# Kernel tuning notes

Hardware: AMD Instinct MI355X
Metric: run time of the kernel (lower is better)

## Reference

```python
import jax, jax.numpy as jnp
import numpy as np

N = 50000   # nodes
E = 1600000 # edges
G = 256     # graphs
EPS = 1e-5  # batchnorm eps (torch default)


def _bn(h, g, b):
    # training-mode BatchNorm1d: biased batch stats
    m = h.mean(0)
    v = h.var(0)
    return (h - m) * jax.lax.rsqrt(v + EPS) * g + b


def _mlp(h, W1, b1, g, be, W2, b2):
    # Lin -> BN -> ReLU -> Lin
    h = jax.nn.relu(_bn(h @ W1 + b1, g, be))
    return h @ W2 + b2


def _scatter_mean(v, idx, n):
    s = jax.ops.segment_sum(v, idx, num_segments=n)
    c = jax.ops.segment_sum(jnp.ones((v.shape[0], 1), v.dtype), idx, num_segments=n)
    return s / jnp.maximum(c, 1.0)


def setup_inputs() -> dict:
    key = jax.random.key(0)
    ks = iter(jax.random.split(key, 32))
    d = {}
    d["x"] = jax.random.normal(next(ks), (N, 48), dtype=jnp.float32)
    d["edge_index"] = jax.random.randint(next(ks), (2, E), 0, N, dtype=jnp.int64)
    d["batch"] = jnp.sort(jax.random.randint(next(ks), (N,), 0, G, dtype=jnp.int64))

    def lin(k, fin, fout):
        kw, kb = jax.random.split(k)
        s = 1.0 / np.sqrt(fin)
        return (jax.random.uniform(kw, (fin, fout), jnp.float32, -s, s),
                jax.random.uniform(kb, (fout,), jnp.float32, -s, s))

    # input BatchNorm1d(48)
    d["bn_g"] = jnp.ones((48,), jnp.float32)
    d["bn_b"] = jnp.zeros((48,), jnp.float32)

    def mlp_params(prefix, fin, fmid, fout):
        W1, b1 = lin(next(ks), fin, fmid)
        W2, b2 = lin(next(ks), fmid, fout)
        d[prefix + "_W1"], d[prefix + "_b1"] = W1, b1
        d[prefix + "_g"] = jnp.ones((fmid,), jnp.float32)
        d[prefix + "_be"] = jnp.zeros((fmid,), jnp.float32)
        d[prefix + "_W2"], d[prefix + "_b2"] = W2, b2

    mlp_params("e", 96, 128, 128)    # EdgeBlock
    mlp_params("n1", 176, 128, 128)  # NodeBlock mlp1
    mlp_params("n2", 176, 128, 128)  # NodeBlock mlp2
    mlp_params("gl", 128, 128, 2)    # GlobalBlock
    return d


def reference(x, edge_index, batch, bn_g, bn_b,
              e_W1, e_b1, e_g, e_be, e_W2, e_b2,
              n1_W1, n1_b1, n1_g, n1_be, n1_W2, n1_b2,
              n2_W1, n2_b1, n2_g, n2_be, n2_W2, n2_b2,
              gl_W1, gl_b1, gl_g, gl_be, gl_W2, gl_b2):
    x = _bn(x, bn_g, bn_b)
    row, col = edge_index[0], edge_index[1]
    # EdgeBlock: cat(src, dest) -> MLP
    edge_attr = _mlp(jnp.concatenate([x[row], x[col]], axis=1),
                     e_W1, e_b1, e_g, e_be, e_W2, e_b2)
    # NodeBlock: cat(x[row], edge_attr) -> mlp1 -> scatter_mean(col) -> cat(x,.) -> mlp2
    m = _mlp(jnp.concatenate([x[row], edge_attr], axis=1),
             n1_W1, n1_b1, n1_g, n1_be, n1_W2, n1_b2)
    agg = _scatter_mean(m, col, N)
    x2 = _mlp(jnp.concatenate([x, agg], axis=1),
              n2_W1, n2_b1, n2_g, n2_be, n2_W2, n2_b2)
    # GlobalBlock: scatter_mean over graphs -> MLP -> [G, 2]
    u = _scatter_mean(x2, batch, G)
    u = _mlp(u, gl_W1, gl_b1, gl_g, gl_be, gl_W2, gl_b2)
    return u
```

## Files before the change

kernel.cpp:

```cpp
#include <hip/hip_runtime.h>
#include <hip/hip_bf16.h>
#include <stdint.h>

#define DEV static __device__ __forceinline__

constexpr int N_ = 50000;
constexpr int E_ = 1600000;
constexpr int G_ = 256;

typedef __attribute__((ext_vector_type(8))) short short8;
typedef __attribute__((ext_vector_type(4))) float float4v;

DEV uint16_t f2bf(float f){
  uint32_t u = __float_as_uint(f);
  uint32_t r = (u + 0x7fffu + ((u >> 16) & 1u)) >> 16;
  return (uint16_t)r;
}
DEV float bf2f(uint16_t v){ return __uint_as_float((uint32_t)v << 16); }
DEV void unpack2(uint32_t p, float& a, float& b){
  a = __uint_as_float(p << 16);
  b = __uint_as_float(p & 0xffff0000u);
}
DEV uint32_t pack2(float a, float b){
  return (uint32_t)f2bf(a) | ((uint32_t)f2bf(b) << 16);
}
DEV short8 lds_load8(const uint16_t* p){
  union { short8 v; uint2 u[2]; } c;
  c.u[0] = *(const uint2*)p;
  c.u[1] = *(const uint2*)(p + 4);
  return c.v;
}
DEV void lds_store16B_as8(uint32_t* d, uint4 v){
  *(uint2*)d       = make_uint2(v.x, v.y);
  *(uint2*)(d + 2) = make_uint2(v.z, v.w);
}

__global__ __launch_bounds__(256) void k_xstats(const float* __restrict__ x, float* __restrict__ xstats){
  __shared__ float lst[96];
  int t = threadIdx.x;
  if (t < 96) lst[t] = 0.f;
  __syncthreads();
  int gid = blockIdx.x * 256 + t;
  int c4 = (gid % 12) * 4;
  float s[4] = {0,0,0,0}, q[4] = {0,0,0,0};
  const float4v* x4 = (const float4v*)x;
  for (int i = gid; i < N_ * 12; i += 64512){
    float4v v = x4[i];
    #pragma unroll
    for (int j = 0; j < 4; j++){ s[j] += v[j]; q[j] += v[j]*v[j]; }
  }
  #pragma unroll
  for (int j = 0; j < 4; j++){
    atomicAdd(&lst[c4 + j], s[j]);
    atomicAdd(&lst[48 + c4 + j], q[j]);
  }
  __syncthreads();
  if (t < 96) atomicAdd(&xstats[t], lst[t]);
}

__global__ void k_xfin(const float* __restrict__ xstats, const float* __restrict__ g,
                       const float* __restrict__ b, float* __restrict__ sx, float* __restrict__ tx){
  int c = threadIdx.x;
  if (c < 48){
    float m = xstats[c] / (float)N_;
    float v = xstats[48 + c] / (float)N_ - m*m;
    float s = g[c] / sqrtf(v + 1e-5f);
    sx[c] = s; tx[c] = b[c] - m*s;
  }
}

__global__ __launch_bounds__(256) void k_hist(const int* __restrict__ ei, int* __restrict__ counts){
  int e = blockIdx.x * 256 + threadIdx.x;
  if (e < E_) atomicAdd(&counts[ei[E_ + e]], 1);
}

__global__ __launch_bounds__(256) void k_invc(const int* __restrict__ counts, float* __restrict__ invc){
  int n = blockIdx.x * 256 + threadIdx.x;
  if (n < N_){ int c = counts[n]; invc[n] = (c > 0) ? 1.f/(float)c : 0.f; }
}

__global__ __launch_bounds__(256) void k_scanA(const int* __restrict__ counts, int* __restrict__ bsum){
  __shared__ int ws[4];
  int b = blockIdx.x, t = threadIdx.x, lane = t & 63, w = t >> 6;
  int i0 = b*1024 + t*4;
  int s = 0;
  #pragma unroll
  for (int j = 0; j < 4; j++){ int i = i0 + j; if (i < N_) s += counts[i]; }
  for (int d = 1; d < 64; d <<= 1) s += __shfl_xor(s, d);
  if (lane == 0) ws[w] = s;
  __syncthreads();
  if (t == 0) bsum[b] = ws[0] + ws[1] + ws[2] + ws[3];
}
__global__ void k_scanB(const int* __restrict__ bsum, int* __restrict__ boff, int* __restrict__ off, int nb){
  int t = threadIdx.x;
  int v = (t < nb) ? bsum[t] : 0;
  int x = v;
  for (int d = 1; d < 64; d <<= 1){ int y = __shfl_up(x, d); if (t >= d) x += y; }
  if (t < nb) boff[t] = x - v;
  if (t == 63) off[N_] = x;
}
__global__ __launch_bounds__(256) void k_scanC(const int* __restrict__ counts, const int* __restrict__ boff,
                                               int* __restrict__ off, int* __restrict__ cur){
  __shared__ int ws[4];
  int b = blockIdx.x, t = threadIdx.x, lane = t & 63, w = t >> 6;
  int i0 = b*1024 + t*4;
  int v0 = (i0+0 < N_) ? counts[i0+0] : 0;
  int v1 = (i0+1 < N_) ? counts[i0+1] : 0;
  int v2 = (i0+2 < N_) ? counts[i0+2] : 0;
  int v3 = (i0+3 < N_) ? counts[i0+3] : 0;
  int ts = v0+v1+v2+v3, xs = ts;
  for (int d = 1; d < 64; d <<= 1){ int y = __shfl_up(xs, d); if (lane >= d) xs += y; }
  if (lane == 63) ws[w] = xs;
  __syncthreads();
  int woff = 0;
  for (int k = 0; k < w; k++) woff += ws[k];
  int excl = xs - ts + woff + boff[b];
  int e0 = excl, e1 = e0+v0, e2 = e1+v1, e3 = e2+v2;
  if (i0+0 < N_){ off[i0+0] = e0; cur[i0+0] = e0; }
  if (i0+1 < N_){ off[i0+1] = e1; cur[i0+1] = e1; }
  if (i0+2 < N_){ off[i0+2] = e2; cur[i0+2] = e2; }
  if (i0+3 < N_){ off[i0+3] = e3; cur[i0+3] = e3; }
}

__global__ __launch_bounds__(256) void k_place(const int* __restrict__ ei, int* __restrict__ cur,
                                               int2* __restrict__ rcs){
  int e = blockIdx.x * 256 + threadIdx.x;
  if (e < E_){
    int c = ei[E_ + e];
    int p = atomicAdd(&cur[c], 1);
    rcs[p] = make_int2(ei[e], c);
  }
}

__global__ __launch_bounds__(256) void k_wprep(
    const float* __restrict__ eW2, const float* __restrict__ n1W1,
    const float* __restrict__ n1W2, const float* __restrict__ n2W1,
    const float* __restrict__ n2W2, const float* __restrict__ glW1,
    const float* __restrict__ n1b2, const float* __restrict__ n2b2,
    uint16_t* __restrict__ Mt, float* __restrict__ Wcomb,
    float* __restrict__ M3, float* __restrict__ c1, float* __restrict__ c3){
  int flat = blockIdx.x * 256 + threadIdx.x;
  if (flat < 16384){
    int n = flat & 127, k = flat >> 7;
    float a = 0.f;
    for (int j = 0; j < 128; j++) a += eW2[k*128 + j] * n1W1[(48 + j)*128 + n];
    Mt[n*128 + k] = f2bf(a);
  } else if (flat < 32768){
    int b = flat - 16384;
    int n = b & 127, j = b >> 7;
    float a = 0.f;
    for (int m = 0; m < 128; m++) a += n1W2[j*128 + m] * n2W1[(48 + m)*128 + n];
    Wcomb[(48 + j)*128 + n] = a;
  } else if (flat < 38912){
    int b = flat - 32768;
    int n = b & 127, k = b >> 7;
    Wcomb[k*128 + n] = n2W1[k*128 + n];
  } else if (flat < 55296){
    int b = flat - 38912;
    int n = b & 127, j = b >> 7;
    float a = 0.f;
    for (int m = 0; m < 128; m++) a += n2W2[j*128 + m] * glW1[m*128 + n];
    M3[j*128 + n] = a;
  } else if (flat < 55552){
    int e = flat - 55296;
    if (e < 128){
      float a = 0.f;
      for (int m = 0; m < 128; m++) a += n1b2[m] * n2W1[(48 + m)*128 + e];
      c1[e] = a;
    } else {
      int n = e - 128;
      float a = 0.f;
      for (int m = 0; m < 128; m++) a += n2b2[m] * glW1[m*128 + n];
      c3[n] = a;
    }
  }
}

__global__ __launch_bounds__(256) void k_nodegemm(
    const float* __restrict__ x, const float* __restrict__ sx, const float* __restrict__ tx,
    const float* __restrict__ eW1, const float* __restrict__ n1W1,
    uint16_t* __restrict__ AC, uint16_t* __restrict__ Bn){
  __shared__ float xT[48][36];
  __shared__ float W[48][128];
  int t = threadIdx.x;
  int n0 = blockIdx.x * 32;
  for (int idx = t; idx < 384; idx += 256){
    int r = idx / 12, q = idx % 12;
    int n = n0 + r;
    float4v v = {0.f,0.f,0.f,0.f};
    if (n < N_) v = *(const float4v*)&x[(size_t)n*48 + q*4];
    #pragma unroll
    for (int i = 0; i < 4; i++){
      int k = q*4 + i;
      xT[k][r] = v[i] * sx[k] + tx[k];
    }
  }
  int cg = t & 31, ng = t >> 5;
  const float* Wsrc0 = eW1;
  const float* Wsrc1 = eW1 + 48*128;
  const float* Wsrc2 = n1W1;
  for (int seg = 0; seg < 3; seg++){
    const float* Wsrc = (seg == 0) ? Wsrc0 : (seg == 1) ? Wsrc1 : Wsrc2;
    __syncthreads();
    {
      const float4v* src4 = (const float4v*)Wsrc;
      float4v* W4 = (float4v*)W;
      for (int idx = t; idx < 1536; idx += 256) W4[idx] = src4[idx];
    }
    __syncthreads();
    float acc[4][4] = {{0.f}};
    #pragma unroll 4
    for (int k = 0; k < 48; k++){
      float4v xv = *(const float4v*)&xT[k][ng*4];
      float4v wv = *(const float4v*)&W[k][cg*4];
      #pragma unroll
      for (int i = 0; i < 4; i++)
        #pragma unroll
        for (int j = 0; j < 4; j++)
          acc[i][j] += xv[i]*wv[j];
    }
    #pragma unroll
    for (int i = 0; i < 4; i++){
      int n = n0 + ng*4 + i;
      if (n >= N_) continue;
      uint2 pv;
      pv.x = pack2(acc[i][0], acc[i][1]);
      pv.y = pack2(acc[i][2], acc[i][3]);
      if (seg == 0)      *(uint2*)&AC[(size_t)n*256 + cg*4] = pv;
      else if (seg == 1) *(uint2*)&Bn[(size_t)n*128 + cg*4] = pv;
      else               *(uint2*)&AC[(size_t)n*256 + 128 + cg*4] = pv;
    }
  }
}

__global__ __launch_bounds__(256) void k_estats(const int2* __restrict__ rcs,
    const uint16_t* __restrict__ AC, const uint16_t* __restrict__ Bn, float* __restrict__ estR){
  __shared__ float red[4][64][4];
  __shared__ float lst[256];
  int t = threadIdx.x, lane = t & 63, w = t >> 6;
  int wid = blockIdx.x * 4 + w, nw = gridDim.x * 4;
  float s0=0,q0=0,s1=0,q1=0;
  const uint32_t* ACu = (const uint32_t*)AC;
  const uint32_t* Bu  = (const uint32_t*)Bn;
  for (int e = wid; e < E_; e += nw){
    int2 rc = rcs[e];
    uint32_t pa = ACu[(size_t)rc.x*128 + lane];
    uint32_t pb = Bu[(size_t)rc.y*64 + lane];
    float a0,a1,b0,b1; unpack2(pa,a0,a1); unpack2(pb,b0,b1);
    float h0 = a0 + b0, h1 = a1 + b1;
    s0 += h0; q0 += h0*h0; s1 += h1; q1 += h1*h1;
  }
  red[w][lane][0]=s0; red[w][lane][1]=q0; red[w][lane][2]=s1; red[w][lane][3]=q1;
  __syncthreads();
  if (t < 64){
    float S0=0,Q0=0,S1=0,Q1=0;
    for (int ww = 0; ww < 4; ww++){ S0+=red[ww][t][0]; Q0+=red[ww][t][1]; S1+=red[ww][t][2]; Q1+=red[ww][t][3]; }
    lst[2*t] = S0; lst[2*t+1] = S1; lst[128+2*t] = Q0; lst[128+2*t+1] = Q1;
  }
  __syncthreads();
  atomicAdd(&estR[(blockIdx.x & 63)*256 + t], lst[t]);
}

__global__ void k_bnfin(const float* __restrict__ statsR, int reps, const float* __restrict__ g,
                        const float* __restrict__ be, float* __restrict__ s_out, float* __restrict__ t_out,
                        float inv_n){
  int c = threadIdx.x;
  if (c >= 128) return;
  float sm = 0.f, sq = 0.f;
  for (int r = 0; r < reps; r++){ sm += statsR[r*256 + c]; sq += statsR[r*256 + 128 + c]; }
  float m = sm * inv_n;
  float v = sq * inv_n - m*m;
  float s = g[c] / sqrtf(v + 1e-5f);
  s_out[c] = s;
  t_out[c] = be[c] - m*s;
}


__global__ __launch_bounds__(256) void k_epass0(
    const int2* __restrict__ rcs,
    const uint16_t* __restrict__ AC, const uint16_t* __restrict__ Bn,
    const uint16_t* __restrict__ Mt, const float* __restrict__ se, const float* __restrict__ te,
    float* __restrict__ n1R){
  __shared__ __align__(16) uint16_t bufA[64*132];
  __shared__ __align__(16) uint16_t bufB[128*132];
  __shared__ __align__(16) float sete[256];
  __shared__ float lst[256];
  const int t = threadIdx.x;
  const long i0 = (long)blockIdx.x * 64;
  const int lane = t & 63, w = t >> 6;
  const int m = lane & 15, quad = lane >> 4;
  const int e = t >> 2, q = t & 3;

  int2 rc = rcs[i0 + e];
  const uint4* Ap = (const uint4*)((const uint32_t*)AC + (size_t)rc.x*128 + q*16);
  const uint4* Bp = (const uint4*)((const uint32_t*)Bn + (size_t)rc.y*64  + q*16);
  const uint4* Cp = (const uint4*)((const uint32_t*)AC + (size_t)rc.x*128 + 64 + q*16);
  uint4 va0 = Ap[0], va1 = Ap[1], va2 = Ap[2], va3 = Ap[3];
  uint4 vb0 = Bp[0], vb1 = Bp[1], vb2 = Bp[2], vb3 = Bp[3];
  uint4 vc0 = Cp[0], vc1 = Cp[1], vc2 = Cp[2], vc3 = Cp[3];

  if (t < 128){ sete[t] = se[t]; sete[128 + t] = te[t]; }
  lst[t] = 0.f;
  __syncthreads();

  {
    uint32_t* dstd = (uint32_t*)bufA + e*66 + q*16;
    int cb = q*32;
    uint4 vas[4] = {va0, va1, va2, va3};
    uint4 vbs[4] = {vb0, vb1, vb2, vb3};
    #pragma unroll
    for (int u = 0; u < 4; u++){
      uint4 va = vas[u], vb = vbs[u];
      float4v sA = *(const float4v*)&sete[cb + u*8];
      float4v sB = *(const float4v*)&sete[cb + u*8 + 4];
      float4v tA = *(const float4v*)&sete[128 + cb + u*8];
      float4v tB = *(const float4v*)&sete[128 + cb + u*8 + 4];
      float a0,a1,b0,b1; uint4 o;
      unpack2(va.x,a0,a1); unpack2(vb.x,b0,b1);
      o.x = pack2(fmaxf(0.f,(a0+b0)*sA[0]+tA[0]), fmaxf(0.f,(a1+b1)*sA[1]+tA[1]));
      unpack2(va.y,a0,a1); unpack2(vb.y,b0,b1);
      o.y = pack2(fmaxf(0.f,(a0+b0)*sA[2]+tA[2]), fmaxf(0.f,(a1+b1)*sA[3]+tA[3]));
      unpack2(va.z,a0,a1); unpack2(vb.z,b0,b1);
      o.z = pack2(fmaxf(0.f,(a0+b0)*sB[0]+tB[0]), fmaxf(0.f,(a1+b1)*sB[1]+tB[1]));
      unpack2(va.w,a0,a1); unpack2(vb.w,b0,b1);
      o.w = pack2(fmaxf(0.f,(a0+b0)*sB[2]+tB[2]), fmaxf(0.f,(a1+b1)*sB[3]+tB[3]));
      lds_store16B_as8(dstd + u*4, o);
    }
  }
  {
    int n = t >> 1, h = t & 1;
    const uint4* src = (const uint4*)((const uint32_t*)Mt + n*64 + h*32);
    uint32_t* dstd = (uint32_t*)bufB + n*66 + h*32;
    #pragma unroll
    for (int u = 0; u < 8; u++) lds_store16B_as8(dstd + u*4, src[u]);
  }
  __syncthreads();

  float4v acc[8];
  #pragma unroll
  for (int nt = 0; nt < 8; nt++){ acc[nt][0]=0.f; acc[nt][1]=0.f; acc[nt][2]=0.f; acc[nt][3]=0.f; }
  {
    const uint16_t* aptr = bufA + (w*16 + m)*132 + quad*8;
    const uint16_t* bbase = bufB + m*132 + quad*8;
    #pragma unroll
    for (int ks = 0; ks < 4; ks++){
      short8 af = lds_load8(aptr + ks*32);
      #pragma unroll
      for (int nt = 0; nt < 8; nt++){
        short8 bf = lds_load8(bbase + nt*16*132 + ks*32);
        acc[nt] = __builtin_amdgcn_mfma_f32_16x16x32_bf16(af, bf, acc[nt], 0, 0, 0);
      }
    }
  }
  __syncthreads();

  {
    uint32_t* dstd = (uint32_t*)bufA + e*66 + q*16;
    lds_store16B_as8(dstd + 0,  vc0);
    lds_store16B_as8(dstd + 4,  vc1);
    lds_store16B_as8(dstd + 8,  vc2);
    lds_store16B_as8(dstd + 12, vc3);
  }
  #pragma unroll
  for (int nt = 0; nt < 8; nt++)
    #pragma unroll
    for (int reg = 0; reg < 4; reg++)
      bufB[(w*16 + quad*4 + reg)*132 + nt*16 + m] = f2bf(acc[nt][reg]);
  __syncthreads();

  {
    int cp = t & 63, eg = t >> 6;
    float ss0=0,qq0=0,ss1=0,qq1=0;
    #pragma unroll
    for (int it = 0; it < 16; it++){
      int ee = it*4 + eg;
      uint32_t ph = ((uint32_t*)bufB)[ee*66 + cp];
      uint32_t pc = ((uint32_t*)bufA)[ee*66 + cp];
      float h0,h1,c0,c1v;
      unpack2(ph,h0,h1); unpack2(pc,c0,c1v);
      float v0 = h0 + c0, v1 = h1 + c1v;
      ss0 += v0; qq0 += v0*v0; ss1 += v1; qq1 += v1*v1;
    }
    atomicAdd(&lst[2*cp], ss0);
    atomicAdd(&lst[2*cp+1], ss1);
    atomicAdd(&lst[128+2*cp], qq0);
    atomicAdd(&lst[128+2*cp+1], qq1);
  }
  __syncthreads();
  atomicAdd(&n1R[(blockIdx.x & 63)*256 + t], lst[t]);
}

__global__ __launch_bounds__(256) void k_epass1(
    const int2* __restrict__ rcs,
    const uint16_t* __restrict__ AC, const uint16_t* __restrict__ Bn,
    const uint16_t* __restrict__ Mt, const float* __restrict__ se, const float* __restrict__ te,
    const float* __restrict__ sn1, const float* __restrict__ tn1,
    float* __restrict__ aggf){
  __shared__ __align__(16) uint16_t bufA[64*132];
  __shared__ __align__(16) uint16_t bufB[128*132];
  __shared__ __align__(16) float sete[256];
  __shared__ int ssid_s[64], scseg_s[64];
  __shared__ int snseg;
  const int t = threadIdx.x;
  const long i0 = (long)blockIdx.x * 64;
  const int lane = t & 63, w = t >> 6;
  const int m = lane & 15, quad = lane >> 4;
  const int e = t >> 2, q = t & 3;

  uint32_t* bufBu = (uint32_t*)bufB;
  float* segacc = (float*)(bufBu + 4224);

  int2 rc = rcs[i0 + e];
  const uint4* Ap = (const uint4*)((const uint32_t*)AC + (size_t)rc.x*128 + q*16);
  const uint4* Bp = (const uint4*)((const uint32_t*)Bn + (size_t)rc.y*64  + q*16);
  const uint4* Cp = (const uint4*)((const uint32_t*)AC + (size_t)rc.x*128 + 64 + q*16);
  uint4 va0 = Ap[0], va1 = Ap[1], va2 = Ap[2], va3 = Ap[3];
  uint4 vb0 = Bp[0], vb1 = Bp[1], vb2 = Bp[2], vb3 = Bp[3];
  uint4 vc0 = Cp[0], vc1 = Cp[1], vc2 = Cp[2], vc3 = Cp[3];

  if (t < 128){ sete[t] = se[t]; sete[128 + t] = te[t]; }
  if (t < 64){
    int myc = rcs[i0 + t].y;
    int prevc = (t > 0) ? rcs[i0 + t - 1].y : myc;
    bool bnd = (t > 0) && (myc != prevc);
    unsigned long long mask = __ballot(bnd);
    int sid = __popcll(mask << (63 - t));
    ssid_s[t] = sid;
    if (bnd || t == 0) scseg_s[sid] = myc;
    if (t == 63) snseg = sid + 1;
  }
  __syncthreads();

  {
    uint32_t* dstd = (uint32_t*)bufA + e*66 + q*16;
    int cb = q*32;
    uint4 vas[4] = {va0, va1, va2, va3};
    uint4 vbs[4] = {vb0, vb1, vb2, vb3};
    #pragma unroll
    for (int u = 0; u < 4; u++){
      uint4 va = vas[u], vb = vbs[u];
      float4v sA = *(const float4v*)&sete[cb + u*8];
      float4v sB = *(const float4v*)&sete[cb + u*8 + 4];
      float4v tA = *(const float4v*)&sete[128 + cb + u*8];
      float4v tB = *(const float4v*)&sete[128 + cb + u*8 + 4];
      float a0,a1,b0,b1; uint4 o;
      unpack2(va.x,a0,a1); unpack2(vb.x,b0,b1);
      o.x = pack2(fmaxf(0.f,(a0+b0)*sA[0]+tA[0]), fmaxf(0.f,(a1+b1)*sA[1]+tA[1]));
      unpack2(va.y,a0,a1); unpack2(vb.y,b0,b1);
      o.y = pack2(fmaxf(0.f,(a0+b0)*sA[2]+tA[2]), fmaxf(0.f,(a1+b1)*sA[3]+tA[3]));
      unpack2(va.z,a0,a1); unpack2(vb.z,b0,b1);
      o.z = pack2(fmaxf(0.f,(a0+b0)*sB[0]+tB[0]), fmaxf(0.f,(a1+b1)*sB[1]+tB[1]));
      unpack2(va.w,a0,a1); unpack2(vb.w,b0,b1);
      o.w = pack2(fmaxf(0.f,(a0+b0)*sB[2]+tB[2]), fmaxf(0.f,(a1+b1)*sB[3]+tB[3]));
      lds_store16B_as8(dstd + u*4, o);
    }
  }
  {
    int n = t >> 1, h = t & 1;
    const uint4* src = (const uint4*)((const uint32_t*)Mt + n*64 + h*32);
    uint32_t* dstd = bufBu + n*66 + h*32;
    #pragma unroll
    for (int u = 0; u < 8; u++) lds_store16B_as8(dstd + u*4, src[u]);
  }
  __syncthreads();

  float4v acc[8];
  #pragma unroll
  for (int nt = 0; nt < 8; nt++){ acc[nt][0]=0.f; acc[nt][1]=0.f; acc[nt][2]=0.f; acc[nt][3]=0.f; }
  {
    const uint16_t* aptr = bufA + (w*16 + m)*132 + quad*8;
    const uint16_t* bbase = bufB + m*132 + quad*8;
    #pragma unroll
    for (int ks = 0; ks < 4; ks++){
      short8 af = lds_load8(aptr + ks*32);
      #pragma unroll
      for (int nt = 0; nt < 8; nt++){
        short8 bf = lds_load8(bbase + nt*16*132 + ks*32);
        acc[nt] = __builtin_amdgcn_mfma_f32_16x16x32_bf16(af, bf, acc[nt], 0, 0, 0);
      }
    }
  }
  __syncthreads();

  {
    uint32_t* dstd = (uint32_t*)bufA + e*66 + q*16;
    lds_store16B_as8(dstd + 0,  vc0);
    lds_store16B_as8(dstd + 4,  vc1);
    lds_store16B_as8(dstd + 8,  vc2);
    lds_store16B_as8(dstd + 12, vc3);
  }
  #pragma unroll
  for (int nt = 0; nt < 8; nt++)
    #pragma unroll
    for (int reg = 0; reg < 4; reg++)
      bufB[(w*16 + quad*4 + reg)*132 + nt*16 + m] = f2bf(acc[nt][reg]);
  if (t < 128){ sete[t] = sn1[t]; sete[128 + t] = tn1[t]; }
  for (int i = t; i < 24*128; i += 256) segacc[i] = 0.f;
  __syncthreads();

  {
    int cp = t & 63, eg = t >> 6;
    float s0 = sete[2*cp], s1 = sete[2*cp+1];
    float b0 = sete[128+2*cp], b1 = sete[128+2*cp+1];
    int nseg = snseg;
    bool lp = (nseg <= 24);
    int cursid = ssid_s[eg*16];
    float r0 = 0.f, r1 = 0.f;
    for (int it = 0; it < 16; it++){
      int ee = eg*16 + it;
      uint32_t ph = bufBu[ee*66 + cp];
      uint32_t pc = ((uint32_t*)bufA)[ee*66 + cp];
      float h0,h1,c0,c1v;
      unpack2(ph,h0,h1); unpack2(pc,c0,c1v);
      float v0 = fmaxf(0.f, (h0+c0)*s0 + b0);
      float v1 = fmaxf(0.f, (h1+c1v)*s1 + b1);
      int sid = ssid_s[ee];
      if (sid != cursid){
        if (lp){ atomicAdd(&segacc[cursid*128 + 2*cp], r0); atomicAdd(&segacc[cursid*128 + 2*cp+1], r1); }
        else { int c = scseg_s[cursid];
               atomicAdd(&aggf[(size_t)c*128 + 2*cp], r0); atomicAdd(&aggf[(size_t)c*128 + 2*cp+1], r1); }
        cursid = sid; r0 = 0.f; r1 = 0.f;
      }
      r0 += v0; r1 += v1;
    }
    if (lp){ atomicAdd(&segacc[cursid*128 + 2*cp], r0); atomicAdd(&segacc[cursid*128 + 2*cp+1], r1); }
    else { int c = scseg_s[cursid];
           atomicAdd(&aggf[(size_t)c*128 + 2*cp], r0); atomicAdd(&aggf[(size_t)c*128 + 2*cp+1], r1); }
    __syncthreads();
    if (lp){
      for (int idx = t; idx < nseg*64; idx += 256){
        int s = idx >> 6, cpp = idx & 63;
        float v0 = segacc[s*128 + 2*cpp], v1 = segacc[s*128 + 2*cpp+1];
        int c = scseg_s[s];
        float* dst = &aggf[(size_t)c*128 + 2*cpp];
        if (s == 0 || s == nseg - 1){ atomicAdd(dst, v0); atomicAdd(dst+1, v1); }
        else { dst[0] = v0; dst[1] = v1; }
      }
    }
  }
}

__global__ __launch_bounds__(256) void k_n2(const float* __restrict__ x,
    const float* __restrict__ sx, const float* __restrict__ tx,
    const float* __restrict__ aggf, const float* __restrict__ invc,
    const float* __restrict__ Wc, const float* __restrict__ c1, const int* __restrict__ counts,
    float* __restrict__ hn2, float* __restrict__ n2R){
  __shared__ float xT[44][36];
  __shared__ float wT[44][128];
  __shared__ float lst[256];
  int t = threadIdx.x;
  int n0 = blockIdx.x * 32;
  int cg = t & 31, ng = t >> 5;
  lst[t] = 0.f;
  float acc[4][4] = {{0.f}};
  for (int kc = 0; kc < 176; kc += 44){
    __syncthreads();
    for (int idx = t; idx < 32*44; idx += 256){
      int r = idx / 44, k = idx % 44;
      int n = n0 + r, kk = kc + k;
      float v = 0.f;
      if (n < N_){
        if (kk < 48) v = x[(size_t)n*48 + kk] * sx[kk] + tx[kk];
        else         v = aggf[(size_t)n*128 + (kk - 48)] * invc[n];
      }
      xT[k][r] = v;
    }
    for (int idx = t; idx < 44*128; idx += 256){
      int k = idx >> 7, c = idx & 127;
      wT[k][c] = Wc[(kc + k)*128 + c];
    }
    __syncthreads();
    for (int k = 0; k < 44; k++){
      float4v xv = *(const float4v*)&xT[k][ng*4];
      float4v wv = *(const float4v*)&wT[k][cg*4];
      #pragma unroll
      for (int i = 0; i < 4; i++)
        #pragma unroll
        for (int j = 0; j < 4; j++)
          acc[i][j] += xv[i]*wv[j];
    }
  }
  float csum[4] = {0,0,0,0}, cqs[4] = {0,0,0,0};
  for (int i = 0; i < 4; i++){
    int n = n0 + ng*4 + i;
    if (n >= N_) continue;
    bool ok = counts[n] > 0;
    float4v o;
    #pragma unroll
    for (int j = 0; j < 4; j++){
      float vv = acc[i][j] + (ok ? c1[cg*4 + j] : 0.f);
      o[j] = vv; csum[j] += vv; cqs[j] += vv*vv;
    }
    *(float4v*)&hn2[(size_t)n*128 + cg*4] = o;
  }
  #pragma unroll
  for (int j = 0; j < 4; j++){
    atomicAdd(&lst[cg*4 + j], csum[j]);
    atomicAdd(&lst[128 + cg*4 + j], cqs[j]);
  }
  __syncthreads();
  atomicAdd(&n2R[(blockIdx.x & 63)*256 + t], lst[t]);
}

__global__ void k_goff(const int* __restrict__ batch, int* __restrict__ goff){
  int g = threadIdx.x;
  int lo = 0, hi = N_;
  while (lo < hi){ int mid = (lo + hi) >> 1; if (batch[mid] < g) lo = mid + 1; else hi = mid; }
  goff[g] = lo;
  if (g == 0) goff[256] = N_;
}

__global__ __launch_bounds__(128) void k_gmean(const float* __restrict__ hn2, const int* __restrict__ goff,
    const float* __restrict__ sn2, const float* __restrict__ tn2, float* __restrict__ gmean){
  int g = blockIdx.x, c = threadIdx.x;
  int b = goff[g], e = goff[g+1];
  float s = sn2[c], tt = tn2[c], a = 0.f;
  for (int r = b; r < e; r++) a += fmaxf(0.f, hn2[(size_t)r*128 + c]*s + tt);
  gmean[g*128 + c] = (e > b) ? a/(float)(e - b) : 0.f;
}

__global__ __launch_bounds__(256) void k_hg(const float* __restrict__ gmean, const float* __restrict__ M3,
    const float* __restrict__ c3, const int* __restrict__ goff,
    float* __restrict__ hg, float* __restrict__ gls){
  int idx = blockIdx.x * 256 + threadIdx.x;
  int g = idx >> 7, c = idx & 127;
  float a = 0.f;
  for (int k = 0; k < 128; k++) a += gmean[g*128 + k] * M3[k*128 + c];
  if (goff[g+1] > goff[g]) a += c3[c];
  hg[idx] = a;
  atomicAdd(&gls[c], a);
  atomicAdd(&gls[128 + c], a*a);
}

__global__ __launch_bounds__(256) void k_out(const float* __restrict__ hg, const float* __restrict__ sgl,
    const float* __restrict__ tgl, const float* __restrict__ glW2, const float* __restrict__ glb2,
    float* __restrict__ out){
  int idx = blockIdx.x * 256 + threadIdx.x;
  int g = idx >> 1, o = idx & 1;
  float a = 0.f;
  for (int c = 0; c < 128; c++){
    float r = fmaxf(0.f, hg[g*128 + c]*sgl[c] + tgl[c]);
    a += r * glW2[c*2 + o];
  }
  out[idx] = a + glb2[o];
}

extern "C" void kernel_launch(void* const* d_in, const int* in_sizes, int n_in,
                              void* d_out, int out_size, void* d_ws, size_t ws_size,
                              hipStream_t stream){
  const float* x     = (const float*)d_in[0];
  const int*   ei    = (const int*)d_in[1];
  const int*   batch = (const int*)d_in[2];
  const float* bn_g  = (const float*)d_in[3];
  const float* bn_b  = (const float*)d_in[4];
  const float* eW1   = (const float*)d_in[5];
  const float* e_g   = (const float*)d_in[7];
  const float* e_be  = (const float*)d_in[8];
  const float* eW2   = (const float*)d_in[9];
  const float* n1W1  = (const float*)d_in[11];
  const float* n1_g  = (const float*)d_in[13];
  const float* n1_be = (const float*)d_in[14];
  const float* n1W2  = (const float*)d_in[15];
  const float* n1b2  = (const float*)d_in[16];
  const float* n2W1  = (const float*)d_in[17];
  const float* n2_g  = (const float*)d_in[19];
  const float* n2_be = (const float*)d_in[20];
  const float* n2W2  = (const float*)d_in[21];
  const float* n2b2  = (const float*)d_in[22];
  const float* glW1  = (const float*)d_in[23];
  const float* gl_g  = (const float*)d_in[25];
  const float* gl_be = (const float*)d_in[26];
  const float* glW2  = (const float*)d_in[27];
  const float* glb2  = (const float*)d_in[28];
  float* out = (float*)d_out;

  char* w = (char*)d_ws;
  size_t off = 0;
  auto take = [&](size_t bytes) -> char* {
    char* p = w + off;
    off = (off + bytes + 511) & ~(size_t)511;
    return p;
  };

  const size_t ZONE_WORDS = 96 + 3*64*256 + 256 + N_;
  float* zone   = (float*)take(ZONE_WORDS * 4);
  float* xstats = zone;
  float* estR   = zone + 96;
  float* n1R    = zone + 96 + 64*256;
  float* n2R    = zone + 96 + 2*64*256;
  float* gls    = zone + 96 + 3*64*256;
  int*   counts = (int*)(zone + 96 + 3*64*256 + 256);

  float* sx = (float*)take(48*4);   float* tx = (float*)take(48*4);
  float* se = (float*)take(128*4);  float* te = (float*)take(128*4);
  float* sn1 = (float*)take(128*4); float* tn1 = (float*)take(128*4);
  float* sn2 = (float*)take(128*4); float* tn2 = (float*)take(128*4);
  float* sgl = (float*)take(128*4); float* tgl = (float*)take(128*4);
  float* c1 = (float*)take(128*4);  float* c3 = (float*)take(128*4);
  float* invc  = (float*)take((size_t)N_*4);
  float* Wcomb = (float*)take(176*128*4);
  float* M3    = (float*)take(128*128*4);
  float* gmean = (float*)take(G_*128*4);
  float* hg    = (float*)take(G_*128*4);
  int* offs = (int*)take((N_+1)*4);
  int* cur  = (int*)take(N_*4);
  int* goff = (int*)take(257*4);
  int* bsum = (int*)take(64*4);
  int* boff = (int*)take(64*4);
  uint16_t* Mt = (uint16_t*)take(128*128*2);
  uint16_t* AC = (uint16_t*)take((size_t)N_*256*2);
  uint16_t* Bn = (uint16_t*)take((size_t)N_*128*2);
  float* aggf  = (float*)take((size_t)N_*128*4);
  float* hn2   = (float*)take((size_t)N_*128*4);
  int2* rcs = (int2*)take((size_t)E_*8);

  if (off > ws_size) return;

  hipMemsetAsync(zone, 0, ZONE_WORDS*4, stream);
  hipMemsetAsync(aggf, 0, (size_t)N_*128*4, stream);

  const int NB = (N_ + 1023) / 1024;
  hipLaunchKernelGGL(k_xstats, dim3(252), dim3(256), 0, stream, x, xstats);
  hipLaunchKernelGGL(k_hist, dim3((E_+255)/256), dim3(256), 0, stream, ei, counts);
  hipLaunchKernelGGL(k_xfin, dim3(1), dim3(64), 0, stream, xstats, bn_g, bn_b, sx, tx);
  hipLaunchKernelGGL(k_scanA, dim3(NB), dim3(256), 0, stream, counts, bsum);
  hipLaunchKernelGGL(k_scanB, dim3(1), dim3(64), 0, stream, bsum, boff, offs, NB);
  hipLaunchKernelGGL(k_scanC, dim3(NB), dim3(256), 0, stream, counts, boff, offs, cur);
  hipLaunchKernelGGL(k_place, dim3((E_+255)/256), dim3(256), 0, stream, ei, cur, rcs);
  hipLaunchKernelGGL(k_invc, dim3((N_+255)/256), dim3(256), 0, stream, counts, invc);
  hipLaunchKernelGGL(k_wprep, dim3(217), dim3(256), 0, stream,
                     eW2, n1W1, n1W2, n2W1, n2W2, glW1, n1b2, n2b2, Mt, Wcomb, M3, c1, c3);
  hipLaunchKernelGGL(k_nodegemm, dim3((N_+31)/32), dim3(256), 0, stream,
                     x, sx, tx, eW1, n1W1, AC, Bn);
  hipLaunchKernelGGL(k_estats, dim3(1024), dim3(256), 0, stream, rcs, AC, Bn, estR);
  hipLaunchKernelGGL(k_bnfin, dim3(1), dim3(128), 0, stream, estR, 64, e_g, e_be, se, te, 1.f/(float)E_);
  hipLaunchKernelGGL(k_epass0, dim3(E_/64), dim3(256), 0, stream,
                     rcs, AC, Bn, Mt, se, te, n1R);
  hipLaunchKernelGGL(k_bnfin, dim3(1), dim3(128), 0, stream, n1R, 64, n1_g, n1_be, sn1, tn1, 1.f/(float)E_);
  hipLaunchKernelGGL(k_epass1, dim3(E_/64), dim3(256), 0, stream,
                     rcs, AC, Bn, Mt, se, te, sn1, tn1, aggf);
  hipLaunchKernelGGL(k_n2, dim3((N_+31)/32), dim3(256), 0, stream,
                     x, sx, tx, aggf, invc, Wcomb, c1, counts, hn2, n2R);
  hipLaunchKernelGGL(k_bnfin, dim3(1), dim3(128), 0, stream, n2R, 64, n2_g, n2_be, sn2, tn2, 1.f/(float)N_);
  hipLaunchKernelGGL(k_goff, dim3(1), dim3(256), 0, stream, batch, goff);
  hipLaunchKernelGGL(k_gmean, dim3(256), dim3(128), 0, stream, hn2, goff, sn2, tn2, gmean);
  hipLaunchKernelGGL(k_hg, dim3(128), dim3(256), 0, stream, gmean, M3, c3, goff, hg, gls);
  hipLaunchKernelGGL(k_bnfin, dim3(1), dim3(128), 0, stream, gls, 1, gl_g, gl_be, sgl, tgl, 1.f/(float)G_);
  hipLaunchKernelGGL(k_out, dim3(2), dim3(256), 0, stream, hg, sgl, tgl, glW2, glb2, out);
}
```

Measured before the change: 1.524 ms.

## Recompute per-edge row projections from gathered bf16 node features via MFMA

Node-level precomputed projections (AC, 256 bf16 per node) are replaced by a compact bf16 normalized-feature array (48 per node). Each edge kernel now gathers these 48-wide rows and recomputes the x[row]@W1 and x[row]@n1W1 products with MFMA inside the edge kernels. The dest-side term Bn is loaded once per column segment into LDS. The aim is to cut random-gather bandwidth over 1.6M edges at the cost of extra tensor-core compute in three edge passes. Blocks grow to 128 edges and 512 threads, and the edge-stats pass becomes an MFMA kernel.

```diff
diff --git a/kernel.cpp b/kernel.cpp
--- a/kernel.cpp
+++ b/kernel.cpp
@@ -29,10 +29,6 @@
   c.u[0] = *(const uint2*)p;
   c.u[1] = *(const uint2*)(p + 4);
   return c.v;
-}
-DEV void lds_store16B_as8(uint32_t* d, uint4 v){
-  *(uint2*)d       = make_uint2(v.x, v.y);
-  *(uint2*)(d + 2) = make_uint2(v.z, v.w);
 }
 
 __global__ __launch_bounds__(256) void k_xstats(const float* __restrict__ x, float* __restrict__ xstats){
@@ -133,12 +129,13 @@
 }
 
 __global__ __launch_bounds__(256) void k_wprep(
-    const float* __restrict__ eW2, const float* __restrict__ n1W1,
+    const float* __restrict__ eW1, const float* __restrict__ eW2, const float* __restrict__ n1W1,
     const float* __restrict__ n1W2, const float* __restrict__ n2W1,
     const float* __restrict__ n2W2, const float* __restrict__ glW1,
     const float* __restrict__ n1b2, const float* __restrict__ n2b2,
     uint16_t* __restrict__ Mt, float* __restrict__ Wcomb,
-    float* __restrict__ M3, float* __restrict__ c1, float* __restrict__ c3){
+    float* __restrict__ M3, float* __restrict__ c1, float* __restrict__ c3,
+    uint16_t* __restrict__ W1t, uint16_t* __restrict__ N1t){
   int flat = blockIdx.x * 256 + threadIdx.x;
   if (flat < 16384){
     int n = flat & 127, k = flat >> 7;
@@ -173,13 +170,21 @@
       for (int m = 0; m < 128; m++) a += n2b2[m] * glW1[m*128 + n];
       c3[n] = a;
     }
+  } else if (flat < 63744){
+    int b = flat - 55552;
+    int n = b & 127, k = b >> 7;
+    W1t[n*64 + k] = (k < 48) ? f2bf(eW1[k*128 + n]) : (uint16_t)0;
+  } else if (flat < 71936){
+    int b = flat - 63744;
+    int n = b & 127, j = b >> 7;
+    N1t[n*64 + j] = (j < 48) ? f2bf(n1W1[j*128 + n]) : (uint16_t)0;
   }
 }
 
 __global__ __launch_bounds__(256) void k_nodegemm(
     const float* __restrict__ x, const float* __restrict__ sx, const float* __restrict__ tx,
-    const float* __restrict__ eW1, const float* __restrict__ n1W1,
-    uint16_t* __restrict__ AC, uint16_t* __restrict__ Bn){
+    const float* __restrict__ eW1,
+    uint16_t* __restrict__ Bn, uint16_t* __restrict__ xn){
   __shared__ float xT[48][36];
   __shared__ float W[48][128];
   int t = threadIdx.x;
@@ -189,76 +194,47 @@
     int n = n0 + r;
     float4v v = {0.f,0.f,0.f,0.f};
     if (n < N_) v = *(const float4v*)&x[(size_t)n*48 + q*4];
+    float xv[4];
     #pragma unroll
     for (int i = 0; i < 4; i++){
       int k = q*4 + i;
-      xT[k][r] = v[i] * sx[k] + tx[k];
-    }
-  }
+      xv[i] = v[i] * sx[k] + tx[k];
+      xT[k][r] = xv[i];
+    }
+    if (n < N_){
+      uint2 pv;
+      pv.x = pack2(xv[0], xv[1]);
+      pv.y = pack2(xv[2], xv[3]);
+      *(uint2*)&xn[(size_t)n*48 + q*4] = pv;
+    }
+  }
+  {
+    const float4v* src4 = (const float4v*)(eW1 + 48*128);
+    float4v* W4 = (float4v*)W;
+    for (int idx = t; idx < 1536; idx += 256) W4[idx] = src4[idx];
+  }
+  __syncthreads();
   int cg = t & 31, ng = t >> 5;
-  const float* Wsrc0 = eW1;
-  const float* Wsrc1 = eW1 + 48*128;
-  const float* Wsrc2 = n1W1;
-  for (int seg = 0; seg < 3; seg++){
-    const float* Wsrc = (seg == 0) ? Wsrc0 : (seg == 1) ? Wsrc1 : Wsrc2;
-    __syncthreads();
-    {
-      const float4v* src4 = (const float4v*)Wsrc;
-      float4v* W4 = (float4v*)W;
-      for (int idx = t; idx < 1536; idx += 256) W4[idx] = src4[idx];
-    }
-    __syncthreads();
-    float acc[4][4] = {{0.f}};
-    #pragma unroll 4
-    for (int k = 0; k < 48; k++){
-      float4v xv = *(const float4v*)&xT[k][ng*4];
-      float4v wv = *(const float4v*)&W[k][cg*4];
-      #pragma unroll
-      for (int i = 0; i < 4; i++)
-        #pragma unroll
-        for (int j = 0; j < 4; j++)
-          acc[i][j] += xv[i]*wv[j];
-    }
-    #pragma unroll
-    for (int i = 0; i < 4; i++){
-      int n = n0 + ng*4 + i;
-      if (n >= N_) continue;
-      uint2 pv;
-      pv.x = pack2(acc[i][0], acc[i][1]);
-      pv.y = pack2(acc[i][2], acc[i][3]);
-      if (seg == 0)      *(uint2*)&AC[(size_t)n*256 + cg*4] = pv;
-      else if (seg == 1) *(uint2*)&Bn[(size_t)n*128 + cg*4] = pv;
-      else               *(uint2*)&AC[(size_t)n*256 + 128 + cg*4] = pv;
-    }
-  }
-}
-
-__global__ __launch_bounds__(256) void k_estats(const int2* __restrict__ rcs,
-    const uint16_t* __restrict__ AC, const uint16_t* __restrict__ Bn, float* __restrict__ estR){
-  __shared__ float red[4][64][4];
-  __shared__ float lst[256];
-  int t = threadIdx.x, lane = t & 63, w = t >> 6;
-  int wid = blockIdx.x * 4 + w, nw = gridDim.x * 4;
-  float s0=0,q0=0,s1=0,q1=0;
-  const uint32_t* ACu = (const uint32_t*)AC;
-  const uint32_t* Bu  = (const uint32_t*)Bn;
-  for (int e = wid; e < E_; e += nw){
-    int2 rc = rcs[e];
-    uint32_t pa = ACu[(size_t)rc.x*128 + lane];
-    uint32_t pb = Bu[(size_t)rc.y*64 + lane];
-    float a0,a1,b0,b1; unpack2(pa,a0,a1); unpack2(pb,b0,b1);
-    float h0 = a0 + b0, h1 = a1 + b1;
-    s0 += h0; q0 += h0*h0; s1 += h1; q1 += h1*h1;
-  }
-  red[w][lane][0]=s0; red[w][lane][1]=q0; red[w][lane][2]=s1; red[w][lane][3]=q1;
-  __syncthreads();
-  if (t < 64){
-    float S0=0,Q0=0,S1=0,Q1=0;
-    for (int ww = 0; ww < 4; ww++){ S0+=red[ww][t][0]; Q0+=red[ww][t][1]; S1+=red[ww][t][2]; Q1+=red[ww][t][3]; }
-    lst[2*t] = S0; lst[2*t+1] = S1; lst[128+2*t] = Q0; lst[128+2*t+1] = Q1;
-  }
-  __syncthreads();
-  atomicAdd(&estR[(blockIdx.x & 63)*256 + t], lst[t]);
+  float acc[4][4] = {{0.f}};
+  #pragma unroll 4
+  for (int k = 0; k < 48; k++){
+    float4v xv = *(const float4v*)&xT[k][ng*4];
+    float4v wv = *(const float4v*)&W[k][cg*4];
+    #pragma unroll
+    for (int i = 0; i < 4; i++)
+      #pragma unroll
+      for (int j = 0; j < 4; j++)
+        acc[i][j] += xv[i]*wv[j];
+  }
+  #pragma unroll
+  for (int i = 0; i < 4; i++){
+    int n = n0 + ng*4 + i;
+    if (n >= N_) continue;
+    uint2 pv;
+    pv.x = pack2(acc[i][0], acc[i][1]);
+    pv.y = pack2(acc[i][2], acc[i][3]);
+    *(uint2*)&Bn[(size_t)n*128 + cg*4] = pv;
+  }
 }
 
 __global__ void k_bnfin(const float* __restrict__ statsR, int reps, const float* __restrict__ g,
@@ -276,63 +252,72 @@
 }
 
 
-__global__ __launch_bounds__(256) void k_epass0(
-    const int2* __restrict__ rcs,
-    const uint16_t* __restrict__ AC, const uint16_t* __restrict__ Bn,
-    const uint16_t* __restrict__ Mt, const float* __restrict__ se, const float* __restrict__ te,
-    float* __restrict__ n1R){
-  __shared__ __align__(16) uint16_t bufA[64*132];
-  __shared__ __align__(16) uint16_t bufB[128*132];
-  __shared__ __align__(16) float sete[256];
+__global__ __launch_bounds__(512, 4) void k_estats2(
+    const int2* __restrict__ rcs, const uint16_t* __restrict__ xn,
+    const uint16_t* __restrict__ Bn, const uint16_t* __restrict__ W1t,
+    float* __restrict__ estR){
+  __shared__ __align__(16) uint16_t XNR[128*68];
+  __shared__ __align__(16) uint16_t Hh[128*132];
+  __shared__ __align__(16) uint16_t Wb[128*68];
+  __shared__ __align__(16) uint16_t Bseg[32*128];
   __shared__ float lst[256];
+  __shared__ int ssid[128], scol[128], scseg[32];
+  __shared__ int sm_w0, snseg;
   const int t = threadIdx.x;
-  const long i0 = (long)blockIdx.x * 64;
+  const long i0 = (long)blockIdx.x * 128;
   const int lane = t & 63, w = t >> 6;
   const int m = lane & 15, quad = lane >> 4;
-  const int e = t >> 2, q = t & 3;
-
-  int2 rc = rcs[i0 + e];
-  const uint4* Ap = (const uint4*)((const uint32_t*)AC + (size_t)rc.x*128 + q*16);
-  const uint4* Bp = (const uint4*)((const uint32_t*)Bn + (size_t)rc.y*64  + q*16);
-  const uint4* Cp = (const uint4*)((const uint32_t*)AC + (size_t)rc.x*128 + 64 + q*16);
-  uint4 va0 = Ap[0], va1 = Ap[1], va2 = Ap[2], va3 = Ap[3];
-  uint4 vb0 = Bp[0], vb1 = Bp[1], vb2 = Bp[2], vb3 = Bp[3];
-  uint4 vc0 = Cp[0], vc1 = Cp[1], vc2 = Cp[2], vc3 = Cp[3];
-
-  if (t < 128){ sete[t] = se[t]; sete[128 + t] = te[t]; }
-  lst[t] = 0.f;
-  __syncthreads();
-
-  {
-    uint32_t* dstd = (uint32_t*)bufA + e*66 + q*16;
-    int cb = q*32;
-    uint4 vas[4] = {va0, va1, va2, va3};
-    uint4 vbs[4] = {vb0, vb1, vb2, vb3};
-    #pragma unroll
-    for (int u = 0; u < 4; u++){
-      uint4 va = vas[u], vb = vbs[u];
-      float4v sA = *(const float4v*)&sete[cb + u*8];
-      float4v sB = *(const float4v*)&sete[cb + u*8 + 4];
-      float4v tA = *(const float4v*)&sete[128 + cb + u*8];
-      float4v tB = *(const float4v*)&sete[128 + cb + u*8 + 4];
-      float a0,a1,b0,b1; uint4 o;
-      unpack2(va.x,a0,a1); unpack2(vb.x,b0,b1);
-      o.x = pack2(fmaxf(0.f,(a0+b0)*sA[0]+tA[0]), fmaxf(0.f,(a1+b1)*sA[1]+tA[1]));
-      unpack2(va.y,a0,a1); unpack2(vb.y,b0,b1);
-      o.y = pack2(fmaxf(0.f,(a0+b0)*sA[2]+tA[2]), fmaxf(0.f,(a1+b1)*sA[3]+tA[3]));
-      unpack2(va.z,a0,a1); unpack2(vb.z,b0,b1);
-      o.z = pack2(fmaxf(0.f,(a0+b0)*sB[0]+tB[0]), fmaxf(0.f,(a1+b1)*sB[1]+tB[1]));
-      unpack2(va.w,a0,a1); unpack2(vb.w,b0,b1);
-      o.w = pack2(fmaxf(0.f,(a0+b0)*sB[2]+tB[2]), fmaxf(0.f,(a1+b1)*sB[3]+tB[3]));
-      lds_store16B_as8(dstd + u*4, o);
-    }
-  }
-  {
-    int n = t >> 1, h = t & 1;
-    const uint4* src = (const uint4*)((const uint32_t*)Mt + n*64 + h*32);
-    uint32_t* dstd = (uint32_t*)bufB + n*66 + h*32;
-    #pragma unroll
-    for (int u = 0; u < 8; u++) lds_store16B_as8(dstd + u*4, src[u]);
+  uint32_t* XNRd = (uint32_t*)XNR;
+  uint32_t* Wd = (uint32_t*)Wb;
+  uint32_t* Hd = (uint32_t*)Hh;
+
+  if (t < 256) lst[t] = 0.f;
+
+  int sid_loc = 0; bool bnd = false; int myc = 0;
+  if (t < 128){
+    myc = rcs[i0 + t].y;
+    int prevc = (t > 0) ? rcs[i0 + t - 1].y : myc;
+    bnd = (t > 0) && (myc != prevc);
+    unsigned long long mask = __ballot(bnd);
+    sid_loc = __popcll(mask << (63 - lane));
+    scol[t] = myc;
+    if (t == 63) sm_w0 = sid_loc;
+  }
+  {
+    int e = t >> 2, q = t & 3;
+    int r = rcs[i0 + e].x;
+    const uint2* src = (const uint2*)(xn + (size_t)r*48 + q*12);
+    uint2 d0 = src[0], d1 = src[1], d2 = src[2];
+    uint32_t* dst = XNRd + e*34 + q*6;
+    *(uint2*)dst = d0; *(uint2*)(dst+2) = d1; *(uint2*)(dst+4) = d2;
+  }
+  for (int idx = t; idx < 1024; idx += 512){
+    int rr = idx >> 3;
+    XNRd[rr*34 + 24 + (idx & 7)] = 0;
+  }
+  {
+    const uint32_t* src = (const uint32_t*)W1t;
+    for (int idx = t; idx < 4096; idx += 512){
+      int n = idx >> 5, d = idx & 31;
+      Wd[n*34 + d] = src[n*32 + d];
+    }
+  }
+  __syncthreads();
+  if (t >= 64 && t < 128) sid_loc += sm_w0;
+  if (t < 128){
+    ssid[t] = sid_loc;
+    if ((bnd || t == 0) && sid_loc < 32) scseg[sid_loc] = myc;
+    if (t == 127) snseg = sid_loc + 1;
+  }
+  __syncthreads();
+  {
+    int ns = snseg; if (ns > 32) ns = 32;
+    uint32_t* Bsegd = (uint32_t*)Bseg;
+    const uint32_t* Bnd = (const uint32_t*)Bn;
+    for (int idx = t; idx < ns*64; idx += 512){
+      int s = idx >> 6, d = idx & 63;
+      Bsegd[s*64 + d] = Bnd[(size_t)scseg[s]*64 + d];
+    }
   }
   __syncthreads();
 
@@ -340,46 +325,44 @@
   #pragma unroll
   for (int nt = 0; nt < 8; nt++){ acc[nt][0]=0.f; acc[nt][1]=0.f; acc[nt][2]=0.f; acc[nt][3]=0.f; }
   {
-    const uint16_t* aptr = bufA + (w*16 + m)*132 + quad*8;
-    const uint16_t* bbase = bufB + m*132 + quad*8;
-    #pragma unroll
-    for (int ks = 0; ks < 4; ks++){
+    const uint16_t* aptr = XNR + (w*16 + m)*68 + quad*8;
+    const uint16_t* bbase = Wb + m*68 + quad*8;
+    #pragma unroll
+    for (int ks = 0; ks < 2; ks++){
       short8 af = lds_load8(aptr + ks*32);
       #pragma unroll
       for (int nt = 0; nt < 8; nt++){
-        short8 bf = lds_load8(bbase + nt*16*132 + ks*32);
+        short8 bf = lds_load8(bbase + nt*16*68 + ks*32);
         acc[nt] = __builtin_amdgcn_mfma_f32_16x16x32_bf16(af, bf, acc[nt], 0, 0, 0);
       }
     }
   }
-  __syncthreads();
-
-  {
-    uint32_t* dstd = (uint32_t*)bufA + e*66 + q*16;
-    lds_store16B_as8(dstd + 0,  vc0);
-    lds_store16B_as8(dstd + 4,  vc1);
-    lds_store16B_as8(dstd + 8,  vc2);
-    lds_store16B_as8(dstd + 12, vc3);
-  }
-  #pragma unroll
-  for (int nt = 0; nt < 8; nt++)
-    #pragma unroll
-    for (int reg = 0; reg < 4; reg++)
-      bufB[(w*16 + quad*4 + reg)*132 + nt*16 + m] = f2bf(acc[nt][reg]);
-  __syncthreads();
-
+  {
+    int elb = w*16 + quad*4;
+    int sids[4];
+    #pragma unroll
+    for (int reg = 0; reg < 4; reg++) sids[reg] = ssid[elb + reg];
+    #pragma unroll
+    for (int nt = 0; nt < 8; nt++){
+      int col = nt*16 + m;
+      #pragma unroll
+      for (int reg = 0; reg < 4; reg++){
+        float b = (sids[reg] < 32) ? bf2f(Bseg[sids[reg]*128 + col])
+                                   : bf2f(Bn[(size_t)scol[elb+reg]*128 + col]);
+        Hh[(elb+reg)*132 + col] = f2bf(acc[nt][reg] + b);
+      }
+    }
+  }
+  __syncthreads();
   {
     int cp = t & 63, eg = t >> 6;
     float ss0=0,qq0=0,ss1=0,qq1=0;
     #pragma unroll
     for (int it = 0; it < 16; it++){
-      int ee = it*4 + eg;
-      uint32_t ph = ((uint32_t*)bufB)[ee*66 + cp];
-      uint32_t pc = ((uint32_t*)bufA)[ee*66 + cp];
-      float h0,h1,c0,c1v;
-      unpack2(ph,h0,h1); unpack2(pc,c0,c1v);
-      float v0 = h0 + c0, v1 = h1 + c1v;
-      ss0 += v0; qq0 += v0*v0; ss1 += v1; qq1 += v1*v1;
+      int e = it*8 + eg;
+      uint32_t ph = Hd[e*66 + cp];
+      float h0,h1; unpack2(ph,h0,h1);
+      ss0 += h0; qq0 += h0*h0; ss1 += h1; qq1 += h1*h1;
     }
     atomicAdd(&lst[2*cp], ss0);
     atomicAdd(&lst[2*cp+1], ss1);
@@ -387,80 +370,79 @@
     atomicAdd(&lst[128+2*cp+1], qq1);
   }
   __syncthreads();
-  atomicAdd(&n1R[(blockIdx.x & 63)*256 + t], lst[t]);
-}
-
-__global__ __launch_bounds__(256) void k_epass1(
-    const int2* __restrict__ rcs,
-    const uint16_t* __restrict__ AC, const uint16_t* __restrict__ Bn,
-    const uint16_t* __restrict__ Mt, const float* __restrict__ se, const float* __restrict__ te,
-    const float* __restrict__ sn1, const float* __restrict__ tn1,
-    float* __restrict__ aggf){
-  __shared__ __align__(16) uint16_t bufA[64*132];
-  __shared__ __align__(16) uint16_t bufB[128*132];
-  __shared__ __align__(16) float sete[256];
-  __shared__ int ssid_s[64], scseg_s[64];
-  __shared__ int snseg;
+  if (t < 256) atomicAdd(&estR[(blockIdx.x & 63)*256 + t], lst[t]);
+}
+
+__global__ __launch_bounds__(512, 4) void k_epass0(
+    const int2* __restrict__ rcs, const uint16_t* __restrict__ xn,
+    const uint16_t* __restrict__ Bn, const uint16_t* __restrict__ W1t,
+    const uint16_t* __restrict__ Mt, const uint16_t* __restrict__ N1t,
+    const float* __restrict__ se, const float* __restrict__ te,
+    float* __restrict__ n1R){
+  __shared__ __align__(16) uint16_t XNR[128*68];
+  __shared__ __align__(16) uint16_t Hh[128*132];
+  __shared__ __align__(16) uint16_t Wb[128*68];
+  __shared__ __align__(16) uint16_t Bseg[32*128];
+  __shared__ float sete[256];
+  __shared__ float lst[256];
+  __shared__ int ssid[128], scol[128], scseg[32];
+  __shared__ int sm_w0, snseg;
   const int t = threadIdx.x;
-  const long i0 = (long)blockIdx.x * 64;
+  const long i0 = (long)blockIdx.x * 128;
   const int lane = t & 63, w = t >> 6;
   const int m = lane & 15, quad = lane >> 4;
-  const int e = t >> 2, q = t & 3;
-
-  uint32_t* bufBu = (uint32_t*)bufB;
-  float* segacc = (float*)(bufBu + 4224);
-
-  int2 rc = rcs[i0 + e];
-  const uint4* Ap = (const uint4*)((const uint32_t*)AC + (size_t)rc.x*128 + q*16);
-  const uint4* Bp = (const uint4*)((const uint32_t*)Bn + (size_t)rc.y*64  + q*16);
-  const uint4* Cp = (const uint4*)((const uint32_t*)AC + (size_t)rc.x*128 + 64 + q*16);
-  uint4 va0 = Ap[0], va1 = Ap[1], va2 = Ap[2], va3 = Ap[3];
-  uint4 vb0 = Bp[0], vb1 = Bp[1], vb2 = Bp[2], vb3 = Bp[3];
-  uint4 vc0 = Cp[0], vc1 = Cp[1], vc2 = Cp[2], vc3 = Cp[3];
-
+  uint32_t* XNRd = (uint32_t*)XNR;
+  uint32_t* Wd = (uint32_t*)Wb;
+  uint32_t* Hd = (uint32_t*)Hh;
+
+  if (t < 256) lst[t] = 0.f;
   if (t < 128){ sete[t] = se[t]; sete[128 + t] = te[t]; }
-  if (t < 64){
-    int myc = rcs[i0 + t].y;
+
+  int sid_loc = 0; bool bnd = false; int myc = 0;
+  if (t < 128){
+    myc = rcs[i0 + t].y;
     int prevc = (t > 0) ? rcs[i0 + t - 1].y : myc;
-    bool bnd = (t > 0) && (myc != prevc);
+    bnd = (t > 0) && (myc != prevc);
     unsigned long long mask = __ballot(bnd);
-    int sid = __popcll(mask << (63 - t));
-    ssid_s[t] = sid;
-    if (bnd || t == 0) scseg_s[sid] = myc;
-    if (t == 63) snseg = sid + 1;
-  }
-  __syncthreads();
-
-  {
-    uint32_t* dstd = (uint32_t*)bufA + e*66 + q*16;
-    int cb = q*32;
-    uint4 vas[4] = {va0, va1, va2, va3};
-    uint4 vbs[4] = {vb0, vb1, vb2, vb3};
-    #pragma unroll
-    for (int u = 0; u < 4; u++){
-      uint4 va = vas[u], vb = vbs[u];
-      float4v sA = *(const float4v*)&sete[cb + u*8];
-      float4v sB = *(const float4v*)&sete[cb + u*8 + 4];
-      float4v tA = *(const float4v*)&sete[128 + cb + u*8];
-      float4v tB = *(const float4v*)&sete[128 + cb + u*8 + 4];
-      float a0,a1,b0,b1; uint4 o;
-      unpack2(va.x,a0,a1); unpack2(vb.x,b0,b1);
-      o.x = pack2(fmaxf(0.f,(a0+b0)*sA[0]+tA[0]), fmaxf(0.f,(a1+b1)*sA[1]+tA[1]));
-      unpack2(va.y,a0,a1); unpack2(vb.y,b0,b1);
-      o.y = pack2(fmaxf(0.f,(a0+b0)*sA[2]+tA[2]), fmaxf(0.f,(a1+b1)*sA[3]+tA[3]));
-      unpack2(va.z,a0,a1); unpack2(vb.z,b0,b1);
-      o.z = pack2(fmaxf(0.f,(a0+b0)*sB[0]+tB[0]), fmaxf(0.f,(a1+b1)*sB[1]+tB[1]));
-      unpack2(va.w,a0,a1); unpack2(vb.w,b0,b1);
-      o.w = pack2(fmaxf(0.f,(a0+b0)*sB[2]+tB[2]), fmaxf(0.f,(a1+b1)*sB[3]+tB[3]));
-      lds_store16B_as8(dstd + u*4, o);
-    }
-  }
-  {
-    int n = t >> 1, h = t & 1;
-    const uint4* src = (const uint4*)((const uint32_t*)Mt + n*64 + h*32);
-    uint32_t* dstd = bufBu + n*66 + h*32;
-    #pragma unroll
-    for (int u = 0; u < 8; u++) lds_store16B_as8(dstd + u*4, src[u]);
+    sid_loc = __popcll(mask << (63 - lane));
+    scol[t] = myc;
+    if (t == 63) sm_w0 = sid_loc;
+  }
+  {
+    int e = t >> 2, q = t & 3;
+    int r = rcs[i0 + e].x;
+    const uint2* src = (const uint2*)(xn + (size_t)r*48 + q*12);
+    uint2 d0 = src[0], d1 = src[1], d2 = src[2];
+    uint32_t* dst = XNRd + e*34 + q*6;
+    *(uint2*)dst = d0; *(uint2*)(dst+2) = d1; *(uint2*)(dst+4) = d2;
+  }
+  for (int idx = t; idx < 1024; idx += 512){
+    int rr = idx >> 3;
+    XNRd[rr*34 + 24 + (idx & 7)] = 0;
+  }
+  {
+    const uint32_t* src = (const uint32_t*)W1t;
+    for (int idx = t; idx < 4096; idx += 512){
+      int n = idx >> 5, d = idx & 31;
+      Wd[n*34 + d] = src[n*32 + d];
+    }
+  }
+  __syncthreads();
+  if (t >= 64 && t < 128) sid_loc += sm_w0;
+  if (t < 128){
+    ssid[t] = sid_loc;
+    if ((bnd || t == 0) && sid_loc < 32) scseg[sid_loc] = myc;
+    if (t == 127) snseg = sid_loc + 1;
+  }
+  __syncthreads();
+  {
+    int ns = snseg; if (ns > 32) ns = 32;
+    uint32_t* Bsegd = (uint32_t*)Bseg;
+    const uint32_t* Bnd = (const uint32_t*)Bn;
+    for (int idx = t; idx < ns*64; idx += 512){
+      int s = idx >> 6, d = idx & 63;
+      Bsegd[s*64 + d] = Bnd[(size_t)scseg[s]*64 + d];
+    }
   }
   __syncthreads();
 
@@ -468,34 +450,235 @@
   #pragma unroll
   for (int nt = 0; nt < 8; nt++){ acc[nt][0]=0.f; acc[nt][1]=0.f; acc[nt][2]=0.f; acc[nt][3]=0.f; }
   {
-    const uint16_t* aptr = bufA + (w*16 + m)*132 + quad*8;
-    const uint16_t* bbase = bufB + m*132 + quad*8;
-    #pragma unroll
-    for (int ks = 0; ks < 4; ks++){
+    const uint16_t* aptr = XNR + (w*16 + m)*68 + quad*8;
+    const uint16_t* bbase = Wb + m*68 + quad*8;
+    #pragma unroll
+    for (int ks = 0; ks < 2; ks++){
       short8 af = lds_load8(aptr + ks*32);
       #pragma unroll
       for (int nt = 0; nt < 8; nt++){
-        short8 bf = lds_load8(bbase + nt*16*132 + ks*32);
+        short8 bf = lds_load8(bbase + nt*16*68 + ks*32);
         acc[nt] = __builtin_amdgcn_mfma_f32_16x16x32_bf16(af, bf, acc[nt], 0, 0, 0);
       }
     }
   }
-  __syncthreads();
-
-  {
-    uint32_t* dstd = (uint32_t*)bufA + e*66 + q*16;
-    lds_store16B_as8(dstd + 0,  vc0);
-    lds_store16B_as8(dstd + 4,  vc1);
-    lds_store16B_as8(dstd + 8,  vc2);
-    lds_store16B_as8(dstd + 12, vc3);
-  }
+  {
+    int elb = w*16 + quad*4;
+    int sids[4];
+    #pragma unroll
+    for (int reg = 0; reg < 4; reg++) sids[reg] = ssid[elb + reg];
+    #pragma unroll
+    for (int nt = 0; nt < 8; nt++){
+      int col = nt*16 + m;
+      float sc = sete[col], tc = sete[128 + col];
+      #pragma unroll
+      for (int reg = 0; reg < 4; reg++){
+        float b = (sids[reg] < 32) ? bf2f(Bseg[sids[reg]*128 + col])
+                                   : bf2f(Bn[(size_t)scol[elb+reg]*128 + col]);
+        float v = fmaxf(0.f, (acc[nt][reg] + b)*sc + tc);
+        Hh[(elb+reg)*132 + col] = f2bf(v);
+      }
+    }
+  }
+
+  float4v acc2[8];
   #pragma unroll
-  for (int nt = 0; nt < 8; nt++)
-    #pragma unroll
-    for (int reg = 0; reg < 4; reg++)
-      bufB[(w*16 + quad*4 + reg)*132 + nt*16 + m] = f2bf(acc[nt][reg]);
+  for (int nt = 0; nt < 8; nt++){ acc2[nt][0]=0.f; acc2[nt][1]=0.f; acc2[nt][2]=0.f; acc2[nt][3]=0.f; }
+  const uint32_t* Mtd = (const uint32_t*)Mt;
+  const uint32_t* N1td = (const uint32_t*)N1t;
+  for (int s = 0; s < 3; s++){
+    __syncthreads();
+    for (int idx = t; idx < 4096; idx += 512){
+      int n = idx >> 5, d = idx & 31;
+      Wd[n*34 + d] = (s < 2) ? Mtd[n*64 + s*32 + d] : N1td[n*32 + d];
+    }
+    __syncthreads();
+    const uint16_t* a2 = (s == 2) ? (XNR + (w*16 + m)*68 + quad*8)
+                                  : (Hh + (w*16 + m)*132 + s*64 + quad*8);
+    const uint16_t* bbase = Wb + m*68 + quad*8;
+    #pragma unroll
+    for (int ks = 0; ks < 2; ks++){
+      short8 af = lds_load8(a2 + ks*32);
+      #pragma unroll
+      for (int nt = 0; nt < 8; nt++){
+        short8 bf = lds_load8(bbase + nt*16*68 + ks*32);
+        acc2[nt] = __builtin_amdgcn_mfma_f32_16x16x32_bf16(af, bf, acc2[nt], 0, 0, 0);
+      }
+    }
+  }
+  __syncthreads();
+  {
+    int elb = w*16 + quad*4;
+    #pragma unroll
+    for (int nt = 0; nt < 8; nt++)
+      #pragma unroll
+      for (int reg = 0; reg < 4; reg++)
+        Hh[(elb+reg)*132 + nt*16 + m] = f2bf(acc2[nt][reg]);
+  }
+  __syncthreads();
+  {
+    int cp = t & 63, eg = t >> 6;
+    float ss0=0,qq0=0,ss1=0,qq1=0;
+    #pragma unroll
+    for (int it = 0; it < 16; it++){
+      int e = it*8 + eg;
+      uint32_t ph = Hd[e*66 + cp];
+      float h0,h1; unpack2(ph,h0,h1);
+      ss0 += h0; qq0 += h0*h0; ss1 += h1; qq1 += h1*h1;
+    }
+    atomicAdd(&lst[2*cp], ss0);
+    atomicAdd(&lst[2*cp+1], ss1);
+    atomicAdd(&lst[128+2*cp], qq0);
+    atomicAdd(&lst[128+2*cp+1], qq1);
+  }
+  __syncthreads();
+  if (t < 256) atomicAdd(&n1R[(blockIdx.x & 63)*256 + t], lst[t]);
+}
+
+__global__ __launch_bounds__(512, 4) void k_epass1(
+    const int2* __restrict__ rcs, const uint16_t* __restrict__ xn,
+    const uint16_t* __restrict__ Bn, const uint16_t* __restrict__ W1t,
+    const uint16_t* __restrict__ Mt, const uint16_t* __restrict__ N1t,
+    const float* __restrict__ se, const float* __restrict__ te,
+    const float* __restrict__ sn1, const float* __restrict__ tn1,
+    float* __restrict__ aggf){
+  __shared__ __align__(16) uint16_t XNR[128*68];
+  __shared__ __align__(16) uint16_t Hh[128*132];
+  __shared__ __align__(16) uint16_t Wb[128*68];
+  __shared__ __align__(16) uint16_t Bseg[32*128];
+  __shared__ float sete[256];
+  __shared__ int ssid[128], scol[128], scseg[32];
+  __shared__ int sm_w0, snseg;
+  const int t = threadIdx.x;
+  const long i0 = (long)blockIdx.x * 128;
+  const int lane = t & 63, w = t >> 6;
+  const int m = lane & 15, quad = lane >> 4;
+  uint32_t* XNRd = (uint32_t*)XNR;
+  uint32_t* Wd = (uint32_t*)Wb;
+  uint32_t* Hd = (uint32_t*)Hh;
+  float* segacc = (float*)Wb;
+
+  if (t < 128){ sete[t] = se[t]; sete[128 + t] = te[t]; }
+
+  int sid_loc = 0; bool bnd = false; int myc = 0;
+  if (t < 128){
+    myc = rcs[i0 + t].y;
+    int prevc = (t > 0) ? rcs[i0 + t - 1].y : myc;
+    bnd = (t > 0) && (myc != prevc);
+    unsigned long long mask = __ballot(bnd);
+    sid_loc = __popcll(mask << (63 - lane));
+    scol[t] = myc;
+    if (t == 63) sm_w0 = sid_loc;
+  }
+  {
+    int e = t >> 2, q = t & 3;
+    int r = rcs[i0 + e].x;
+    const uint2* src = (const uint2*)(xn + (size_t)r*48 + q*12);
+    uint2 d0 = src[0], d1 = src[1], d2 = src[2];
+    uint32_t* dst = XNRd + e*34 + q*6;
+    *(uint2*)dst = d0; *(uint2*)(dst+2) = d1; *(uint2*)(dst+4) = d2;
+  }
+  for (int idx = t; idx < 1024; idx += 512){
+    int rr = idx >> 3;
+    XNRd[rr*34 + 24 + (idx & 7)] = 0;
+  }
+  {
+    const uint32_t* src = (const uint32_t*)W1t;
+    for (int idx = t; idx < 4096; idx += 512){
+      int n = idx >> 5, d = idx & 31;
+      Wd[n*34 + d] = src[n*32 + d];
+    }
+  }
+  __syncthreads();
+  if (t >= 64 && t < 128) sid_loc += sm_w0;
+  if (t < 128){
+    ssid[t] = sid_loc;
+    if ((bnd || t == 0) && sid_loc < 32) scseg[sid_loc] = myc;
+    if (t == 127) snseg = sid_loc + 1;
+  }
+  __syncthreads();
+  {
+    int ns = snseg; if (ns > 32) ns = 32;
+    uint32_t* Bsegd = (uint32_t*)Bseg;
+    const uint32_t* Bnd = (const uint32_t*)Bn;
+    for (int idx = t; idx < ns*64; idx += 512){
+      int s = idx >> 6, d = idx & 63;
+      Bsegd[s*64 + d] = Bnd[(size_t)scseg[s]*64 + d];
+    }
+  }
+  __syncthreads();
+
+  float4v acc[8];
+  #pragma unroll
+  for (int nt = 0; nt < 8; nt++){ acc[nt][0]=0.f; acc[nt][1]=0.f; acc[nt][2]=0.f; acc[nt][3]=0.f; }
+  {
+    const uint16_t* aptr = XNR + (w*16 + m)*68 + quad*8;
+    const uint16_t* bbase = Wb + m*68 + quad*8;
+    #pragma unroll
+    for (int ks = 0; ks < 2; ks++){
+      short8 af = lds_load8(aptr + ks*32);
+      #pragma unroll
+      for (int nt = 0; nt < 8; nt++){
+        short8 bf = lds_load8(bbase + nt*16*68 + ks*32);
+        acc[nt] = __builtin_amdgcn_mfma_f32_16x16x32_bf16(af, bf, acc[nt], 0, 0, 0);
+      }
+    }
+  }
+  {
+    int elb = w*16 + quad*4;
+    int sids[4];
+    #pragma unroll
+    for (int reg = 0; reg < 4; reg++) sids[reg] = ssid[elb + reg];
+    #pragma unroll
+    for (int nt = 0; nt < 8; nt++){
+      int col = nt*16 + m;
+      float sc = sete[col], tc = sete[128 + col];
+      #pragma unroll
+      for (int reg = 0; reg < 4; reg++){
+        float b = (sids[reg] < 32) ? bf2f(Bseg[sids[reg]*128 + col])
+                                   : bf2f(Bn[(size_t)scol[elb+reg]*128 + col]);
+        float v = fmaxf(0.f, (acc[nt][reg] + b)*sc + tc);
+        Hh[(elb+reg)*132 + col] = f2bf(v);
+      }
+    }
+  }
+
+  float4v acc2[8];
+  #pragma unroll
+  for (int nt = 0; nt < 8; nt++){ acc2[nt][0]=0.f; acc2[nt][1]=0.f; acc2[nt][2]=0.f; acc2[nt][3]=0.f; }
+  const uint32_t* Mtd = (const uint32_t*)Mt;
+  const uint32_t* N1td = (const uint32_t*)N1t;
+  for (int s = 0; s < 3; s++){
+    __syncthreads();
+    for (int idx = t; idx < 4096; idx += 512){
+      int n = idx >> 5, d = idx & 31;
+      Wd[n*34 + d] = (s < 2) ? Mtd[n*64 + s*32 + d] : N1td[n*32 + d];
+    }
+    __syncthreads();
+    const uint16_t* a2 = (s == 2) ? (XNR + (w*16 + m)*68 + quad*8)
+                                  : (Hh + (w*16 + m)*132 + s*64 + quad*8);
+    const uint16_t* bbase = Wb + m*68 + quad*8;
+    #pragma unroll
+    for (int ks = 0; ks < 2; ks++){
+      short8 af = lds_load8(a2 + ks*32);
+      #pragma unroll
+      for (int nt = 0; nt < 8; nt++){
+        short8 bf = lds_load8(bbase + nt*16*68 + ks*32);
+        acc2[nt] = __builtin_amdgcn_mfma_f32_16x16x32_bf16(af, bf, acc2[nt], 0, 0, 0);
+      }
+    }
+  }
+  __syncthreads();
+  {
+    int elb = w*16 + quad*4;
+    #pragma unroll
+    for (int nt = 0; nt < 8; nt++)
+      #pragma unroll
+      for (int reg = 0; reg < 4; reg++)
+        Hh[(elb+reg)*132 + nt*16 + m] = f2bf(acc2[nt][reg]);
+  }
   if (t < 128){ sete[t] = sn1[t]; sete[128 + t] = tn1[t]; }
-  for (int i = t; i < 24*128; i += 256) segacc[i] = 0.f;
+  for (int idx = t; idx < 32*128; idx += 512) segacc[idx] = 0.f;
   __syncthreads();
 
   {
@@ -503,35 +686,32 @@
     float s0 = sete[2*cp], s1 = sete[2*cp+1];
     float b0 = sete[128+2*cp], b1 = sete[128+2*cp+1];
     int nseg = snseg;
-    bool lp = (nseg <= 24);
-    int cursid = ssid_s[eg*16];
+    bool lp = (nseg <= 32);
+    int cursid = ssid[eg*16];
+    int curcol = scol[eg*16];
     float r0 = 0.f, r1 = 0.f;
     for (int it = 0; it < 16; it++){
-      int ee = eg*16 + it;
-      uint32_t ph = bufBu[ee*66 + cp];
-      uint32_t pc = ((uint32_t*)bufA)[ee*66 + cp];
-      float h0,h1,c0,c1v;
-      unpack2(ph,h0,h1); unpack2(pc,c0,c1v);
-      float v0 = fmaxf(0.f, (h0+c0)*s0 + b0);
-      float v1 = fmaxf(0.f, (h1+c1v)*s1 + b1);
-      int sid = ssid_s[ee];
+      int e = eg*16 + it;
+      uint32_t ph = Hd[e*66 + cp];
+      float h0,h1; unpack2(ph,h0,h1);
+      float v0 = fmaxf(0.f, h0*s0 + b0);
+      float v1 = fmaxf(0.f, h1*s1 + b1);
+      int sid = ssid[e];
       if (sid != cursid){
         if (lp){ atomicAdd(&segacc[cursid*128 + 2*cp], r0); atomicAdd(&segacc[cursid*128 + 2*cp+1], r1); }
-        else { int c = scseg_s[cursid];
-               atomicAdd(&aggf[(size_t)c*128 + 2*cp], r0); atomicAdd(&aggf[(size_t)c*128 + 2*cp+1], r1); }
-        cursid = sid; r0 = 0.f; r1 = 0.f;
+        else { atomicAdd(&aggf[(size_t)curcol*128 + 2*cp], r0); atomicAdd(&aggf[(size_t)curcol*128 + 2*cp+1], r1); }
+        cursid = sid; curcol = scol[e]; r0 = 0.f; r1 = 0.f;
       }
       r0 += v0; r1 += v1;
     }
     if (lp){ atomicAdd(&segacc[cursid*128 + 2*cp], r0); atomicAdd(&segacc[cursid*128 + 2*cp+1], r1); }
-    else { int c = scseg_s[cursid];
-           atomicAdd(&aggf[(size_t)c*128 + 2*cp], r0); atomicAdd(&aggf[(size_t)c*128 + 2*cp+1], r1); }
+    else { atomicAdd(&aggf[(size_t)curcol*128 + 2*cp], r0); atomicAdd(&aggf[(size_t)curcol*128 + 2*cp+1], r1); }
     __syncthreads();
     if (lp){
-      for (int idx = t; idx < nseg*64; idx += 256){
+      for (int idx = t; idx < nseg*64; idx += 512){
         int s = idx >> 6, cpp = idx & 63;
         float v0 = segacc[s*128 + 2*cpp], v1 = segacc[s*128 + 2*cpp+1];
-        int c = scseg_s[s];
+        int c = scseg[s];
         float* dst = &aggf[(size_t)c*128 + 2*cpp];
         if (s == 0 || s == nseg - 1){ atomicAdd(dst, v0); atomicAdd(dst+1, v1); }
         else { dst[0] = v0; dst[1] = v1; }
@@ -707,9 +887,11 @@
   int* goff = (int*)take(257*4);
   int* bsum = (int*)take(64*4);
   int* boff = (int*)take(64*4);
-  uint16_t* Mt = (uint16_t*)take(128*128*2);
-  uint16_t* AC = (uint16_t*)take((size_t)N_*256*2);
-  uint16_t* Bn = (uint16_t*)take((size_t)N_*128*2);
+  uint16_t* Mt  = (uint16_t*)take(128*128*2);
+  uint16_t* W1t = (uint16_t*)take(128*64*2);
+  uint16_t* N1t = (uint16_t*)take(128*64*2);
+  uint16_t* xn  = (uint16_t*)take((size_t)N_*48*2);
+  uint16_t* Bn  = (uint16_t*)take((size_t)N_*128*2);
   float* aggf  = (float*)take((size_t)N_*128*4);
   float* hn2   = (float*)take((size_t)N_*128*4);
   int2* rcs = (int2*)take((size_t)E_*8);
@@ -728,17 +910,19 @@
   hipLaunchKernelGGL(k_scanC, dim3(NB), dim3(256), 0, stream, counts, boff, offs, cur);
   hipLaunchKernelGGL(k_place, dim3((E_+255)/256), dim3(256), 0, stream, ei, cur, rcs);
   hipLaunchKernelGGL(k_invc, dim3((N_+255)/256), dim3(256), 0, stream, counts, invc);
-  hipLaunchKernelGGL(k_wprep, dim3(217), dim3(256), 0, stream,
-                     eW2, n1W1, n1W2, n2W1, n2W2, glW1, n1b2, n2b2, Mt, Wcomb, M3, c1, c3);
+  hipLaunchKernelGGL(k_wprep, dim3(281), dim3(256), 0, stream,
+                     eW1, eW2, n1W1, n1W2, n2W1, n2W2, glW1, n1b2, n2b2,
+                     Mt, Wcomb, M3, c1, c3, W1t, N1t);
   hipLaunchKernelGGL(k_nodegemm, dim3((N_+31)/32), dim3(256), 0, stream,
-                     x, sx, tx, eW1, n1W1, AC, Bn);
-  hipLaunchKernelGGL(k_estats, dim3(1024), dim3(256), 0, stream, rcs, AC, Bn, estR);
+                     x, sx, tx, eW1, Bn, xn);
+  hipLaunchKernelGGL(k_estats2, dim3(E_/128), dim3(512), 0, stream,
+                     rcs, xn, Bn, W1t, estR);
   hipLaunchKernelGGL(k_bnfin, dim3(1), dim3(128), 0, stream, estR, 64, e_g, e_be, se, te, 1.f/(float)E_);
-  hipLaunchKernelGGL(k_epass0, dim3(E_/64), dim3(256), 0, stream,
-                     rcs, AC, Bn, Mt, se, te, n1R);
+  hipLaunchKernelGGL(k_epass0, dim3(E_/128), dim3(512), 0, stream,
+                     rcs, xn, Bn, W1t, Mt, N1t, se, te, n1R);
   hipLaunchKernelGGL(k_bnfin, dim3(1), dim3(128), 0, stream, n1R, 64, n1_g, n1_be, sn1, tn1, 1.f/(float)E_);
-  hipLaunchKernelGGL(k_epass1, dim3(E_/64), dim3(256), 0, stream,
-                     rcs, AC, Bn, Mt, se, te, sn1, tn1, aggf);
+  hipLaunchKernelGGL(k_epass1, dim3(E_/128), dim3(512), 0, stream,
+                     rcs, xn, Bn, W1t, Mt, N1t, se, te, sn1, tn1, aggf);
   hipLaunchKernelGGL(k_n2, dim3((N_+31)/32), dim3(256), 0, stream,
                      x, sx, tx, aggf, invc, Wcomb, c1, counts, hn2, n2R);
   hipLaunchKernelGGL(k_bnfin, dim3(1), dim3(128), 0, stream, n2R, 64, n2_g, n2_be, sn2, tn2, 1.f/(float)N_);
```

After: 1.656 ms. 8.7% more time.
